# Performance work log

Hardware: AMD Instinct MI355X
Metric: run time of the kernel (lower is better)

## Reference

```python
import jax, jax.numpy as jnp
import numpy as np

B, S, D, H = 2, 2048, 1024, 16
HD = D // H  # head_dim = 64


def setup_inputs() -> dict:
    key = jax.random.key(0)
    ks = jax.random.split(key, 12)
    scale = 1.0 / np.sqrt(D)
    inp = {
        "query": jax.random.normal(ks[0], (B, S, D), jnp.float32),
        "key": jax.random.normal(ks[1], (B, S, D), jnp.float32),
        "value": jax.random.normal(ks[2], (B, S, D), jnp.float32),
        # causal mask, True = masked out; shape [B, q_len, k_len]
        "mask": jnp.broadcast_to(
            jnp.triu(jnp.ones((S, S), jnp.bool_), k=1), (B, S, S)
        ),
        "Wq": jax.random.normal(ks[3], (D, D), jnp.float32) * scale,
        "bq": jnp.zeros((D,), jnp.float32),
        "Wk": jax.random.normal(ks[4], (D, D), jnp.float32) * scale,
        "bk": jnp.zeros((D,), jnp.float32),
        "Wv": jax.random.normal(ks[5], (D, D), jnp.float32) * scale,
        "bv": jnp.zeros((D,), jnp.float32),
        "Wo": jax.random.normal(ks[6], (D, D), jnp.float32) * scale,
        "bo": jnp.zeros((D,), jnp.float32),
    }
    return inp


def _split_heads(x):
    b, s, _ = x.shape
    return x.reshape(b, s, H, HD).transpose(0, 2, 1, 3)  # [B,H,S,HD]


def reference(query, key, value, mask, Wq, bq, Wk, bk, Wv, bv, Wo, bo):
    # Linear layers use torch convention: y = x @ W.T + b, W is [out, in]
    q = _split_heads(query @ Wq.T + bq)
    k = _split_heads(key @ Wk.T + bk)
    v = _split_heads(value @ Wv.T + bv)
    scores = jnp.einsum("bhqd,bhkd->bhqk", q, k) / jnp.sqrt(jnp.float32(HD))
    # normalized mask [B,1,q,k]; True means masked
    scores = jnp.where(mask[:, None, :, :], jnp.finfo(scores.dtype).min, scores)
    attn = jax.nn.softmax(scores, axis=-1)  # dropout is identity in eval
    ctx = jnp.einsum("bhqk,bhkd->bhqd", attn, v)
    merged = ctx.transpose(0, 2, 1, 3).reshape(query.shape[0], -1, D)
    out = merged @ Wo.T + bo
    return out
```

## Files before the change

### kernel.cpp

```cpp
#include <hip/hip_runtime.h>

#define B_ 2
#define S_ 2048
#define D_ 1024
#define H_ 16
#define HD_ 64
#define M_ (B_ * S_)

typedef __bf16 bf16x8 __attribute__((ext_vector_type(8)));
typedef float f32x4 __attribute__((ext_vector_type(4)));

__device__ inline unsigned short f2bf(float f) {
    unsigned int u = __builtin_bit_cast(unsigned int, f);
    u += 0x7fffu + ((u >> 16) & 1u);
    return (unsigned short)(u >> 16);
}

__device__ inline void async_ld16(const unsigned short* g, unsigned short* l) {
    __builtin_amdgcn_global_load_lds(
        (const __attribute__((address_space(1))) unsigned int*)g,
        (__attribute__((address_space(3))) unsigned int*)l, 16, 0, 0);
}

template <int CTRL>
__device__ inline float dpp_mov(float v) {
    return __builtin_bit_cast(float,
        __builtin_amdgcn_update_dpp(0, __builtin_bit_cast(int, v), CTRL, 0xF, 0xF, true));
}
__device__ inline float row_max16(float v) {
    v = fmaxf(v, dpp_mov<0xB1>(v));
    v = fmaxf(v, dpp_mov<0x4E>(v));
    v = fmaxf(v, dpp_mov<0x141>(v));
    v = fmaxf(v, dpp_mov<0x140>(v));
    return v;
}
__device__ inline float row_sum16(float v) {
    v += dpp_mov<0xB1>(v);
    v += dpp_mov<0x4E>(v);
    v += dpp_mov<0x141>(v);
    v += dpp_mov<0x140>(v);
    return v;
}

__global__ __launch_bounds__(256) void cvt_all(
    const float* __restrict__ i0, const float* __restrict__ i1, const float* __restrict__ i2,
    const float* __restrict__ i3, const float* __restrict__ i4, const float* __restrict__ i5,
    const float* __restrict__ i6,
    unsigned short* __restrict__ o0, unsigned short* __restrict__ o1, unsigned short* __restrict__ o2,
    unsigned short* __restrict__ o3, unsigned short* __restrict__ o4, unsigned short* __restrict__ o5,
    unsigned short* __restrict__ o6, int nbig, int nsmall) {
    int z = blockIdx.y;
    const float* in = (z == 0) ? i0 : (z == 1) ? i1 : (z == 2) ? i2 : (z == 3) ? i3
                     : (z == 4) ? i4 : (z == 5) ? i5 : i6;
    unsigned short* out = (z == 0) ? o0 : (z == 1) ? o1 : (z == 2) ? o2 : (z == 3) ? o3
                         : (z == 4) ? o4 : (z == 5) ? o5 : o6;
    int n = (z < 3) ? nbig : nsmall;
    int i = (blockIdx.x * 256 + threadIdx.x) * 4;
    if (i >= n) return;
    float4 v = *(const float4*)(in + i);
    ushort4 o;
    o.x = f2bf(v.x); o.y = f2bf(v.y); o.z = f2bf(v.z); o.w = f2bf(v.w);
    *(ushort4*)(out + i) = o;
}

__device__ inline void gemm_compute(const unsigned short* __restrict__ A,
                                    const unsigned short* __restrict__ W,
                                    int K, int m0, int n0,
                                    unsigned short* As0, unsigned short* As1,
                                    unsigned short* Bs0, unsigned short* Bs1,
                                    f32x4 acc[4][4]) {
    const int t = threadIdx.x;
    const int lane = t & 63, wave = t >> 6;
    const int ml = lane & 15, quad = lane >> 4;
    const int wr = (wave >> 1) * 64, wc = (wave & 1) * 64;
    const int lrow = lane >> 3;
    const int gchunk = (lane & 7) ^ lrow;

    const f32x4 zero = {0.f, 0.f, 0.f, 0.f};
    for (int i = 0; i < 4; i++)
        for (int j = 0; j < 4; j++) acc[i][j] = zero;

    const int niter = K >> 6;

    auto issue = [&](int kt, unsigned short* As, unsigned short* Bs) {
        int k0 = kt << 6;
        for (int i = 0; i < 4; i++) {
            int r = wave * 32 + i * 8;
            async_ld16(A + (size_t)(m0 + r + lrow) * K + k0 + gchunk * 8, As + r * 64);
            async_ld16(W + (size_t)(n0 + r + lrow) * K + k0 + gchunk * 8, Bs + r * 64);
        }
    };

    issue(0, As0, Bs0);
    __syncthreads();

    for (int kt = 0; kt < niter; kt++) {
        unsigned short* As = (kt & 1) ? As1 : As0;
        unsigned short* Bs = (kt & 1) ? Bs1 : Bs0;
        if (kt + 1 < niter) issue(kt + 1, (kt & 1) ? As0 : As1, (kt & 1) ? Bs0 : Bs1);

        for (int kk = 0; kk < 2; ++kk) {
            bf16x8 af[4], bfr[4];
            for (int i = 0; i < 4; i++)
                af[i] = *(const bf16x8*)(As + (wr + i * 16 + ml) * 64 + (((kk * 4 + quad) ^ (ml & 7)) << 3));
            for (int j = 0; j < 4; j++)
                bfr[j] = *(const bf16x8*)(Bs + (wc + j * 16 + ml) * 64 + (((kk * 4 + quad) ^ (ml & 7)) << 3));
            for (int i = 0; i < 4; i++)
                for (int j = 0; j < 4; j++)
                    acc[i][j] = __builtin_amdgcn_mfma_f32_16x16x32_bf16(af[i], bfr[j], acc[i][j], 0, 0, 0);
        }
        __syncthreads();
    }
}

__global__ __launch_bounds__(256) void gemm_qkv(
    const unsigned short* __restrict__ xq, const unsigned short* __restrict__ xk,
    const unsigned short* __restrict__ xv,
    const unsigned short* __restrict__ wq, const unsigned short* __restrict__ wk,
    const unsigned short* __restrict__ wv,
    const float* __restrict__ bq, const float* __restrict__ bk, const float* __restrict__ bv,
    unsigned short* __restrict__ oq, unsigned short* __restrict__ ok,
    unsigned short* __restrict__ ov) {
    __shared__ unsigned short As0[128 * 64], As1[128 * 64], Bs0[128 * 64], Bs1[128 * 64];
    const unsigned short *A, *W;
    const float* bias;
    unsigned short* out;
    int z = blockIdx.z;
    if (z == 0) { A = xq; W = wq; bias = bq; out = oq; }
    else if (z == 1) { A = xk; W = wk; bias = bk; out = ok; }
    else { A = xv; W = wv; bias = bv; out = ov; }

    int m0 = blockIdx.y * 128, n0 = blockIdx.x * 128;
    f32x4 acc[4][4];
    gemm_compute(A, W, D_, m0, n0, As0, As1, Bs0, Bs1, acc);

    const int t = threadIdx.x, lane = t & 63, wave = t >> 6;
    const int ml = lane & 15, quad = lane >> 4;
    const int wr = (wave >> 1) * 64, wc = (wave & 1) * 64;
    if (z < 2) {
        for (int i = 0; i < 4; i++)
            for (int j = 0; j < 4; j++) {
                int n = n0 + wc + j * 16 + ml;
                float bb = bias[n];
                int h = n >> 6, d = n & 63;
                for (int rg = 0; rg < 4; rg++) {
                    int m = m0 + wr + i * 16 + quad * 4 + rg;
                    int b = m >> 11, s = m & 2047;
                    out[(((size_t)(b * H_ + h)) * S_ + s) * 64 + d] = f2bf(acc[i][j][rg] + bb);
                }
            }
    } else {
        for (int i = 0; i < 4; i++)
            for (int j = 0; j < 4; j++) {
                int n = n0 + wc + j * 16 + ml;
                float bb = bias[n];
                int h = n >> 6, d = n & 63;
                int m = m0 + wr + i * 16 + quad * 4;
                int b = m >> 11, s = m & 2047;
                ushort4 pk;
                pk.x = f2bf(acc[i][j][0] + bb);
                pk.y = f2bf(acc[i][j][1] + bb);
                pk.z = f2bf(acc[i][j][2] + bb);
                pk.w = f2bf(acc[i][j][3] + bb);
                *(ushort4*)(out + ((size_t)(b * H_ + h) * 64 + d) * S_ + s) = pk;
            }
    }
}

__global__ __launch_bounds__(256) void gemm_out(const unsigned short* __restrict__ A,
                                                const unsigned short* __restrict__ W,
                                                const float* __restrict__ bias,
                                                float* __restrict__ out) {
    __shared__ unsigned short As0[128 * 64], As1[128 * 64], Bs0[128 * 64], Bs1[128 * 64];
    int m0 = blockIdx.y * 128, n0 = blockIdx.x * 128;
    f32x4 acc[4][4];
    gemm_compute(A, W, D_, m0, n0, As0, As1, Bs0, Bs1, acc);

    const int t = threadIdx.x, lane = t & 63, wave = t >> 6;
    const int ml = lane & 15, quad = lane >> 4;
    const int wr = (wave >> 1) * 64, wc = (wave & 1) * 64;
    for (int i = 0; i < 4; i++)
        for (int j = 0; j < 4; j++) {
            int n = n0 + wc + j * 16 + ml;
            float bb = bias[n];
            for (int rg = 0; rg < 4; rg++) {
                int m = m0 + wr + i * 16 + quad * 4 + rg;
                out[(size_t)m * D_ + n] = acc[i][j][rg] + bb;
            }
        }
}

__global__ __launch_bounds__(256, 2) void attn_kernel(const unsigned short* __restrict__ qh,
                                                      const unsigned short* __restrict__ kh,
                                                      const unsigned short* __restrict__ vt,
                                                      unsigned short* __restrict__ ctx) {
    __shared__ unsigned short Ks[2][128 * 64];
    __shared__ unsigned short Vs[2][64 * 128];
    __shared__ unsigned short Ps[64 * 128];

    const int qb = 31 - (blockIdx.x >> 5);
    const int bh = blockIdx.x & 31;
    const size_t base = (size_t)bh * S_ * 64;
    const int t = threadIdx.x, lane = t & 63, wave = t >> 6;
    const int ml = lane & 15, quad = lane >> 4;
    const int lrow = lane >> 3;
    const int gchunk = (lane & 7) ^ lrow;
    const int vrow = lane >> 4;
    const int q0 = qb * 64;

    bf16x8 qf[2];
    {
        int qrow = q0 + wave * 16 + ml;
        qf[0] = *(const bf16x8*)(qh + base + (size_t)qrow * 64 + quad * 8);
        qf[1] = *(const bf16x8*)(qh + base + (size_t)qrow * 64 + 32 + quad * 8);
    }

    const f32x4 zero = {0.f, 0.f, 0.f, 0.f};
    f32x4 acc[4];
    for (int j = 0; j < 4; j++) acc[j] = zero;
    float m_i[4], l_i[4];
    for (int rg = 0; rg < 4; rg++) { m_i[rg] = -INFINITY; l_i[rg] = 0.f; }

    const int ntiles = (qb + 2) >> 1;

    auto issue_tile = [&](int kt, int bb) {
        for (int i = 0; i < 4; i++) {
            int r = wave * 32 + i * 8;
            async_ld16(kh + base + (size_t)(kt * 128 + r + lrow) * 64 + gchunk * 8,
                       Ks[bb] + r * 64);
            int dd = wave * 16 + i * 4;
            int d = dd + vrow;
            async_ld16(vt + base + (size_t)d * S_ + kt * 128 + (((lane & 15) ^ (d & 15)) << 3),
                       Vs[bb] + dd * 128);
        }
    };

    issue_tile(0, 0);
    __syncthreads();

    for (int kt = 0; kt < ntiles; kt++) {
        const int buf = kt & 1;
        if (kt + 1 < ntiles) issue_tile(kt + 1, buf ^ 1);

        f32x4 sacc[8];
        for (int n = 0; n < 8; n++) sacc[n] = zero;
        for (int n = 0; n < 8; n++)
            for (int kk = 0; kk < 2; kk++) {
                bf16x8 kf = *(const bf16x8*)(Ks[buf] + (n * 16 + ml) * 64 +
                                             (((kk * 4 + quad) ^ (ml & 7)) << 3));
                sacc[n] = __builtin_amdgcn_mfma_f32_16x16x32_bf16(qf[kk], kf, sacc[n], 0, 0, 0);
            }

        const float scl = 0.125f;
        const bool last = (kt == ntiles - 1);
        for (int n = 0; n < 8; n++)
            for (int rg = 0; rg < 4; rg++) {
                float sv = sacc[n][rg] * scl;
                if (last) {
                    int kidx = kt * 128 + n * 16 + ml;
                    int qidx = q0 + wave * 16 + quad * 4 + rg;
                    if (kidx > qidx) sv = -3.0e38f;
                }
                sacc[n][rg] = sv;
            }

        float alpha[4];
        for (int rg = 0; rg < 4; rg++) {
            float v = sacc[0][rg];
            for (int n = 1; n < 8; n++) v = fmaxf(v, sacc[n][rg]);
            v = row_max16(v);
            float mo = m_i[rg];
            float mc = fmaxf(mo, v);
            alpha[rg] = __expf(mo - mc);
            m_i[rg] = mc;
        }
        float rsum[4] = {0.f, 0.f, 0.f, 0.f};
        for (int n = 0; n < 8; n++)
            for (int rg = 0; rg < 4; rg++) {
                float p = __expf(sacc[n][rg] - m_i[rg]);
                sacc[n][rg] = p;
                rsum[rg] += p;
            }
        for (int rg = 0; rg < 4; rg++) {
            float v = row_sum16(rsum[rg]);
            l_i[rg] = l_i[rg] * alpha[rg] + v;
            for (int j = 0; j < 4; j++) acc[j][rg] *= alpha[rg];
        }

        const int prow0 = wave * 16;
        for (int n = 0; n < 8; n++)
            for (int rg = 0; rg < 4; rg++) {
                int row = prow0 + quad * 4 + rg;
                int col = n * 16 + ml;
                int c = col >> 3;
                Ps[row * 128 + (((c ^ (row & 7)) & 15) << 3) + (col & 7)] = f2bf(sacc[n][rg]);
            }

        for (int kk = 0; kk < 4; kk++) {
            bf16x8 pf = *(const bf16x8*)(Ps + (prow0 + ml) * 128 +
                                         (((kk * 4 + quad) ^ (ml & 7)) << 3));
            for (int j = 0; j < 4; j++) {
                bf16x8 vf = *(const bf16x8*)(Vs[buf] + (j * 16 + ml) * 128 +
                                             (((kk * 4 + quad) ^ ml) << 3));
                acc[j] = __builtin_amdgcn_mfma_f32_16x16x32_bf16(pf, vf, acc[j], 0, 0, 0);
            }
        }

        __syncthreads();
    }

    int b = bh >> 4, h = bh & 15;
    for (int j = 0; j < 4; j++) {
        int d = j * 16 + ml;
        for (int rg = 0; rg < 4; rg++) {
            int srow = q0 + wave * 16 + quad * 4 + rg;
            float val = acc[j][rg] / l_i[rg];
            ctx[((size_t)(b * S_ + srow)) * D_ + h * 64 + d] = f2bf(val);
        }
    }
}

extern "C" void kernel_launch(void* const* d_in, const int* in_sizes, int n_in,
                              void* d_out, int out_size, void* d_ws, size_t ws_size,
                              hipStream_t stream) {
    const float* query = (const float*)d_in[0];
    const float* key_ = (const float*)d_in[1];
    const float* value = (const float*)d_in[2];
    const float* Wq = (const float*)d_in[4];
    const float* bq = (const float*)d_in[5];
    const float* Wk = (const float*)d_in[6];
    const float* bk = (const float*)d_in[7];
    const float* Wv = (const float*)d_in[8];
    const float* bv = (const float*)d_in[9];
    const float* Wo = (const float*)d_in[10];
    const float* bo = (const float*)d_in[11];
    float* out = (float*)d_out;

    const size_t XE = (size_t)M_ * D_;
    const size_t WE = (size_t)D_ * D_;
    char* ws = (char*)d_ws;
    unsigned short* xq = (unsigned short*)ws; ws += XE * 2;
    unsigned short* xk = (unsigned short*)ws; ws += XE * 2;
    unsigned short* xv = (unsigned short*)ws; ws += XE * 2;
    unsigned short* wqb = (unsigned short*)ws; ws += WE * 2;
    unsigned short* wkb = (unsigned short*)ws; ws += WE * 2;
    unsigned short* wvb = (unsigned short*)ws; ws += WE * 2;
    unsigned short* wob = (unsigned short*)ws; ws += WE * 2;
    unsigned short* qh = (unsigned short*)ws; ws += XE * 2;
    unsigned short* kh = (unsigned short*)ws; ws += XE * 2;
    unsigned short* vt = (unsigned short*)ws; ws += XE * 2;
    unsigned short* ctx = (unsigned short*)ws; ws += XE * 2;

    cvt_all<<<dim3(XE / 1024, 7), 256, 0, stream>>>(
        query, key_, value, Wq, Wk, Wv, Wo,
        xq, xk, xv, wqb, wkb, wvb, wob, (int)XE, (int)WE);

    gemm_qkv<<<dim3(D_ / 128, M_ / 128, 3), 256, 0, stream>>>(
        xq, xk, xv, wqb, wkb, wvb, bq, bk, bv, qh, kh, vt);

    attn_kernel<<<dim3(1024), 256, 0, stream>>>(qh, kh, vt, ctx);

    gemm_out<<<dim3(D_ / 128, M_ / 128), 256, 0, stream>>>(ctx, wob, bo, out);
}
```

Before: 256.7 us.

## Stage QKV epilogue through LDS, compute transposed scores, drop P shared buffer

```diff
diff --git a/kernel.cpp b/kernel.cpp
--- a/kernel.cpp
+++ b/kernel.cpp
@@ -20,26 +20,6 @@
     __builtin_amdgcn_global_load_lds(
         (const __attribute__((address_space(1))) unsigned int*)g,
         (__attribute__((address_space(3))) unsigned int*)l, 16, 0, 0);
-}
-
-template <int CTRL>
-__device__ inline float dpp_mov(float v) {
-    return __builtin_bit_cast(float,
-        __builtin_amdgcn_update_dpp(0, __builtin_bit_cast(int, v), CTRL, 0xF, 0xF, true));
-}
-__device__ inline float row_max16(float v) {
-    v = fmaxf(v, dpp_mov<0xB1>(v));
-    v = fmaxf(v, dpp_mov<0x4E>(v));
-    v = fmaxf(v, dpp_mov<0x141>(v));
-    v = fmaxf(v, dpp_mov<0x140>(v));
-    return v;
-}
-__device__ inline float row_sum16(float v) {
-    v += dpp_mov<0xB1>(v);
-    v += dpp_mov<0x4E>(v);
-    v += dpp_mov<0x141>(v);
-    v += dpp_mov<0x140>(v);
-    return v;
 }
 
 __global__ __launch_bounds__(256) void cvt_all(
@@ -121,7 +101,12 @@
     const float* __restrict__ bq, const float* __restrict__ bk, const float* __restrict__ bv,
     unsigned short* __restrict__ oq, unsigned short* __restrict__ ok,
     unsigned short* __restrict__ ov) {
-    __shared__ unsigned short As0[128 * 64], As1[128 * 64], Bs0[128 * 64], Bs1[128 * 64];
+    extern __shared__ __align__(16) unsigned short smem[];
+    unsigned short* As0 = smem;
+    unsigned short* As1 = smem + 8192;
+    unsigned short* Bs0 = smem + 16384;
+    unsigned short* Bs1 = smem + 24576;
+
     const unsigned short *A, *W;
     const float* bias;
     unsigned short* out;
@@ -137,33 +122,35 @@
     const int t = threadIdx.x, lane = t & 63, wave = t >> 6;
     const int ml = lane & 15, quad = lane >> 4;
     const int wr = (wave >> 1) * 64, wc = (wave & 1) * 64;
+
+    unsigned short* Cs = smem;
+    const float sc = (z == 0) ? 0.125f : 1.0f;
+    for (int i = 0; i < 4; i++)
+        for (int j = 0; j < 4; j++) {
+            int col = wc + j * 16 + ml;
+            float bb = bias[n0 + col];
+            for (int rg = 0; rg < 4; rg++) {
+                int row = wr + i * 16 + quad * 4 + rg;
+                unsigned short v = f2bf((acc[i][j][rg] + bb) * sc);
+                if (z < 2) Cs[row * 136 + col] = v;
+                else       Cs[col * 136 + row] = v;
+            }
+        }
+    __syncthreads();
+
+    const int r = t >> 1, hf = t & 1;
     if (z < 2) {
-        for (int i = 0; i < 4; i++)
-            for (int j = 0; j < 4; j++) {
-                int n = n0 + wc + j * 16 + ml;
-                float bb = bias[n];
-                int h = n >> 6, d = n & 63;
-                for (int rg = 0; rg < 4; rg++) {
-                    int m = m0 + wr + i * 16 + quad * 4 + rg;
-                    int b = m >> 11, s = m & 2047;
-                    out[(((size_t)(b * H_ + h)) * S_ + s) * 64 + d] = f2bf(acc[i][j][rg] + bb);
-                }
-            }
+        unsigned short* dst = out + (size_t)(m0 + r) * D_ + n0 + hf * 64;
+        const unsigned short* src = Cs + r * 136 + hf * 64;
+        for (int i = 0; i < 8; i++)
+            *(uint4*)(dst + i * 8) = *(const uint4*)(src + i * 8);
     } else {
-        for (int i = 0; i < 4; i++)
-            for (int j = 0; j < 4; j++) {
-                int n = n0 + wc + j * 16 + ml;
-                float bb = bias[n];
-                int h = n >> 6, d = n & 63;
-                int m = m0 + wr + i * 16 + quad * 4;
-                int b = m >> 11, s = m & 2047;
-                ushort4 pk;
-                pk.x = f2bf(acc[i][j][0] + bb);
-                pk.y = f2bf(acc[i][j][1] + bb);
-                pk.z = f2bf(acc[i][j][2] + bb);
-                pk.w = f2bf(acc[i][j][3] + bb);
-                *(ushort4*)(out + ((size_t)(b * H_ + h) * 64 + d) * S_ + s) = pk;
-            }
+        int n = n0 + r, h = n >> 6, d = n & 63;
+        int b = m0 >> 11, s0 = m0 & 2047;
+        unsigned short* dst = ov + ((size_t)((b * H_ + h) * 64 + d)) * S_ + s0 + hf * 64;
+        const unsigned short* src = Cs + r * 136 + hf * 64;
+        for (int i = 0; i < 8; i++)
+            *(uint4*)(dst + i * 8) = *(const uint4*)(src + i * 8);
     }
 }
 
@@ -190,17 +177,17 @@
         }
 }
 
-__global__ __launch_bounds__(256, 2) void attn_kernel(const unsigned short* __restrict__ qh,
-                                                      const unsigned short* __restrict__ kh,
+__global__ __launch_bounds__(256, 2) void attn_kernel(const unsigned short* __restrict__ qm,
+                                                      const unsigned short* __restrict__ km,
                                                       const unsigned short* __restrict__ vt,
                                                       unsigned short* __restrict__ ctx) {
     __shared__ unsigned short Ks[2][128 * 64];
     __shared__ unsigned short Vs[2][64 * 128];
-    __shared__ unsigned short Ps[64 * 128];
 
     const int qb = 31 - (blockIdx.x >> 5);
     const int bh = blockIdx.x & 31;
-    const size_t base = (size_t)bh * S_ * 64;
+    const int b = bh >> 4, h = bh & 15;
+    const size_t vbase = (size_t)bh * S_ * 64;
     const int t = threadIdx.x, lane = t & 63, wave = t >> 6;
     const int ml = lane & 15, quad = lane >> 4;
     const int lrow = lane >> 3;
@@ -211,26 +198,26 @@
     bf16x8 qf[2];
     {
         int qrow = q0 + wave * 16 + ml;
-        qf[0] = *(const bf16x8*)(qh + base + (size_t)qrow * 64 + quad * 8);
-        qf[1] = *(const bf16x8*)(qh + base + (size_t)qrow * 64 + 32 + quad * 8);
+        const unsigned short* qp = qm + (size_t)(b * S_ + qrow) * D_ + h * 64;
+        qf[0] = *(const bf16x8*)(qp + quad * 8);
+        qf[1] = *(const bf16x8*)(qp + 32 + quad * 8);
     }
 
     const f32x4 zero = {0.f, 0.f, 0.f, 0.f};
     f32x4 acc[4];
     for (int j = 0; j < 4; j++) acc[j] = zero;
-    float m_i[4], l_i[4];
-    for (int rg = 0; rg < 4; rg++) { m_i[rg] = -INFINITY; l_i[rg] = 0.f; }
+    float m_i = -INFINITY, l_i = 0.f;
 
     const int ntiles = (qb + 2) >> 1;
 
     auto issue_tile = [&](int kt, int bb) {
         for (int i = 0; i < 4; i++) {
             int r = wave * 32 + i * 8;
-            async_ld16(kh + base + (size_t)(kt * 128 + r + lrow) * 64 + gchunk * 8,
+            async_ld16(km + (size_t)(b * S_ + kt * 128 + r + lrow) * D_ + h * 64 + gchunk * 8,
                        Ks[bb] + r * 64);
             int dd = wave * 16 + i * 4;
             int d = dd + vrow;
-            async_ld16(vt + base + (size_t)d * S_ + kt * 128 + (((lane & 15) ^ (d & 15)) << 3),
+            async_ld16(vt + vbase + (size_t)d * S_ + kt * 128 + (((lane & 15) ^ (d & 15)) << 3),
                        Vs[bb] + dd * 128);
         }
     };
@@ -248,73 +235,70 @@
             for (int kk = 0; kk < 2; kk++) {
                 bf16x8 kf = *(const bf16x8*)(Ks[buf] + (n * 16 + ml) * 64 +
                                              (((kk * 4 + quad) ^ (ml & 7)) << 3));
-                sacc[n] = __builtin_amdgcn_mfma_f32_16x16x32_bf16(qf[kk], kf, sacc[n], 0, 0, 0);
-            }
-
-        const float scl = 0.125f;
+                sacc[n] = __builtin_amdgcn_mfma_f32_16x16x32_bf16(kf, qf[kk], sacc[n], 0, 0, 0);
+            }
+
         const bool last = (kt == ntiles - 1);
+        const int qidx = q0 + wave * 16 + ml;
+        if (last) {
+            for (int n = 0; n < 8; n++)
+                for (int rg = 0; rg < 4; rg++) {
+                    int kidx = kt * 128 + n * 16 + quad * 4 + rg;
+                    if (kidx > qidx) sacc[n][rg] = -3.0e38f;
+                }
+        }
+
+        float mx = sacc[0][0];
+        for (int n = 0; n < 8; n++)
+            for (int rg = 0; rg < 4; rg++) mx = fmaxf(mx, sacc[n][rg]);
+        mx = fmaxf(mx, __shfl_xor(mx, 16));
+        mx = fmaxf(mx, __shfl_xor(mx, 32));
+        float mc = fmaxf(m_i, mx);
+        float al = __expf(m_i - mc);
+        m_i = mc;
+        float rs = 0.f;
         for (int n = 0; n < 8; n++)
             for (int rg = 0; rg < 4; rg++) {
-                float sv = sacc[n][rg] * scl;
-                if (last) {
-                    int kidx = kt * 128 + n * 16 + ml;
-                    int qidx = q0 + wave * 16 + quad * 4 + rg;
-                    if (kidx > qidx) sv = -3.0e38f;
-                }
-                sacc[n][rg] = sv;
-            }
-
-        float alpha[4];
-        for (int rg = 0; rg < 4; rg++) {
-            float v = sacc[0][rg];
-            for (int n = 1; n < 8; n++) v = fmaxf(v, sacc[n][rg]);
-            v = row_max16(v);
-            float mo = m_i[rg];
-            float mc = fmaxf(mo, v);
-            alpha[rg] = __expf(mo - mc);
-            m_i[rg] = mc;
-        }
-        float rsum[4] = {0.f, 0.f, 0.f, 0.f};
-        for (int n = 0; n < 8; n++)
+                float p = __expf(sacc[n][rg] - mc);
+                sacc[n][rg] = p;
+                rs += p;
+            }
+        rs += __shfl_xor(rs, 16);
+        rs += __shfl_xor(rs, 32);
+        l_i = l_i * al + rs;
+
+        float alT[4];
+        for (int rg = 0; rg < 4; rg++) alT[rg] = __shfl(al, quad * 4 + rg);
+        for (int j = 0; j < 4; j++)
+            for (int rg = 0; rg < 4; rg++) acc[j][rg] *= alT[rg];
+
+        for (int n2 = 0; n2 < 4; n2++) {
+            union { bf16x8 v; unsigned short u[8]; } pk;
             for (int rg = 0; rg < 4; rg++) {
-                float p = __expf(sacc[n][rg] - m_i[rg]);
-                sacc[n][rg] = p;
-                rsum[rg] += p;
-            }
-        for (int rg = 0; rg < 4; rg++) {
-            float v = row_sum16(rsum[rg]);
-            l_i[rg] = l_i[rg] * alpha[rg] + v;
-            for (int j = 0; j < 4; j++) acc[j][rg] *= alpha[rg];
-        }
-
-        const int prow0 = wave * 16;
-        for (int n = 0; n < 8; n++)
-            for (int rg = 0; rg < 4; rg++) {
-                int row = prow0 + quad * 4 + rg;
-                int col = n * 16 + ml;
-                int c = col >> 3;
-                Ps[row * 128 + (((c ^ (row & 7)) & 15) << 3) + (col & 7)] = f2bf(sacc[n][rg]);
-            }
-
-        for (int kk = 0; kk < 4; kk++) {
-            bf16x8 pf = *(const bf16x8*)(Ps + (prow0 + ml) * 128 +
-                                         (((kk * 4 + quad) ^ (ml & 7)) << 3));
+                pk.u[rg] = f2bf(sacc[2 * n2][rg]);
+                pk.u[4 + rg] = f2bf(sacc[2 * n2 + 1][rg]);
+            }
+            const int c0 = 4 * n2 + (quad >> 1);
+            const int qo = (quad & 1) << 2;
             for (int j = 0; j < 4; j++) {
-                bf16x8 vf = *(const bf16x8*)(Vs[buf] + (j * 16 + ml) * 128 +
-                                             (((kk * 4 + quad) ^ ml) << 3));
-                acc[j] = __builtin_amdgcn_mfma_f32_16x16x32_bf16(pf, vf, acc[j], 0, 0, 0);
+                int row = j * 16 + ml;
+                union { bf16x8 v; uint2 d2[2]; } vv;
+                vv.d2[0] = *(const uint2*)(Vs[buf] + row * 128 + (((c0 ^ (row & 15)) << 3) + qo));
+                vv.d2[1] = *(const uint2*)(Vs[buf] + row * 128 + ((((c0 + 2) ^ (row & 15)) << 3) + qo));
+                acc[j] = __builtin_amdgcn_mfma_f32_16x16x32_bf16(pk.v, vv.v, acc[j], 0, 0, 0);
             }
         }
 
         __syncthreads();
     }
 
-    int b = bh >> 4, h = bh & 15;
+    float lT[4];
+    for (int rg = 0; rg < 4; rg++) lT[rg] = __shfl(l_i, quad * 4 + rg);
     for (int j = 0; j < 4; j++) {
         int d = j * 16 + ml;
         for (int rg = 0; rg < 4; rg++) {
             int srow = q0 + wave * 16 + quad * 4 + rg;
-            float val = acc[j][rg] / l_i[rg];
+            float val = acc[j][rg] / lT[rg];
             ctx[((size_t)(b * S_ + srow)) * D_ + h * 64 + d] = f2bf(val);
         }
     }
@@ -346,8 +330,8 @@
     unsigned short* wkb = (unsigned short*)ws; ws += WE * 2;
     unsigned short* wvb = (unsigned short*)ws; ws += WE * 2;
     unsigned short* wob = (unsigned short*)ws; ws += WE * 2;
-    unsigned short* qh = (unsigned short*)ws; ws += XE * 2;
-    unsigned short* kh = (unsigned short*)ws; ws += XE * 2;
+    unsigned short* qmb = (unsigned short*)ws; ws += XE * 2;
+    unsigned short* kmb = (unsigned short*)ws; ws += XE * 2;
     unsigned short* vt = (unsigned short*)ws; ws += XE * 2;
     unsigned short* ctx = (unsigned short*)ws; ws += XE * 2;
 
@@ -355,10 +339,10 @@
         query, key_, value, Wq, Wk, Wv, Wo,
         xq, xk, xv, wqb, wkb, wvb, wob, (int)XE, (int)WE);
 
-    gemm_qkv<<<dim3(D_ / 128, M_ / 128, 3), 256, 0, stream>>>(
-        xq, xk, xv, wqb, wkb, wvb, bq, bk, bv, qh, kh, vt);
-
-    attn_kernel<<<dim3(1024), 256, 0, stream>>>(qh, kh, vt, ctx);
+    gemm_qkv<<<dim3(D_ / 128, M_ / 128, 3), 256, 65536, stream>>>(
+        xq, xk, xv, wqb, wkb, wvb, bq, bk, bv, qmb, kmb, vt);
+
+    attn_kernel<<<dim3(1024), 256, 0, stream>>>(qmb, kmb, vt, ctx);
 
     gemm_out<<<dim3(D_ / 128, M_ / 128), 256, 0, stream>>>(ctx, wob, bo, out);
 }
```

Result: no change. 255.0 us (-0.7%).
